# Kernel tuning notes

Hardware: AMD Instinct MI355X
Metric: run time of the kernel (lower is better)

The kernel has to match this reference:

```python
import jax, jax.numpy as jnp
import numpy as np

N = 20000       # nodes
E = 262144      # edges
DA, DV, DD = 128, 64, 32
R = 16          # CP rank of TensorProds
NRAD = 8        # radial basis size (hardcoded 8 in module)
R0 = 5.0        # cutoff radius r0


def setup_inputs() -> dict:
    key = jax.random.key(0)
    ks = jax.random.split(key, 13)
    nrm = lambda k, shape, fan: jax.random.normal(k, shape, jnp.float32) / np.sqrt(fan)
    return {
        'r_ij': jax.random.normal(ks[0], (E, 3), jnp.float32),
        'x_a': jax.random.normal(ks[1], (N, DA), jnp.float32),
        'x_v': jax.random.normal(ks[2], (N, DV, 3), jnp.float32),
        'x_d': jax.random.normal(ks[3], (N, DD, 3, 3), jnp.float32),
        'W1_a': nrm(ks[4], (3, R, DA), DA),   # tp_000, tp_011, tp_022 (rank-0 input)
        'W1_v': nrm(ks[5], (4, R, DV), DV),   # tp_101, tp_110, tp_112, tp_121
        'W1_d': nrm(ks[6], (4, R, DD), DD),   # tp_202, tp_211, tp_220, tp_222
        'W2': nrm(ks[7], (11, R, NRAD), NRAD),  # radial-side proj for all 11 TPs
        'Wo_a': nrm(ks[8], (3, DA, R), R),    # outputs of tp_000, tp_110, tp_220
        'Wo_v': nrm(ks[9], (4, DV, R), R),    # outputs of tp_011, tp_101, tp_121, tp_211
        'Wo_d': nrm(ks[10], (4, DD, R), R),   # outputs of tp_022, tp_112, tp_202, tp_222
        'src': jax.random.randint(ks[11], (E,), 0, N),
        'dst': jax.random.randint(ks[12], (E,), 0, N),
    }


def tens_sigmoid_vec(v, eps=1e-6):
    # direction-preserving bounded nonlinearity on rank-1 tensors
    n = jnp.linalg.norm(v, axis=-1, keepdims=True)
    return v * (2.0 * jax.nn.sigmoid(n) - 1.0) / (n + eps)


def _forward(r_ij, x_a, x_v, x_d, W1_a, W1_v, W1_d, W2, Wo_a, Wo_v, Wo_d, src, dst):
    n_nodes = x_a.shape[0]
    # radial_encode_edge(r, 8, r0)
    npi = jnp.pi * jnp.arange(NRAD, dtype=jnp.float32)
    x_sq = jnp.sum(r_ij * r_ij, -1) / R0                       # (E,)
    rad = jnp.cos(npi * jnp.sqrt(x_sq)[:, None]) * jax.nn.relu(1.0 - x_sq)[:, None]  # (E,8)
    rv = tens_sigmoid_vec(r_ij * (17.0 / R0))                  # (E,3)
    phi_a = rad                                                # (E,8)
    phi_v = rad[..., None] * rv[:, None, :]                    # (E,8,3)
    phi_d = rad[..., None, None] * rv[:, None, None, :] * rv[:, None, :, None]  # (E,8,3,3)
    # edges_read_dst: gather node features at destination nodes
    xa_j, xv_j, xd_j = x_a[dst], x_v[dst], x_d[dst]
    p1 = lambda W, x: jnp.einsum('rc,ec...->er...', W, x)      # channel->CP-rank proj
    outp = lambda Wo, t: jnp.einsum('dr,er...->ed...', Wo, t)  # CP-rank->channel proj
    p2a = lambda i: jnp.einsum('rc,ec->er', W2[i], phi_a)
    p2v = lambda i: jnp.einsum('rc,eci->eri', W2[i], phi_v)
    p2d = lambda i: jnp.einsum('rc,ecij->erij', W2[i], phi_d)
    # W2 index order: 000,110,220,011,101,121,211,022,112,202,222
    pa000, pa011, pa022 = p1(W1_a[0], xa_j), p1(W1_a[1], xa_j), p1(W1_a[2], xa_j)
    pv101, pv110, pv112, pv121 = (p1(W1_v[i], xv_j) for i in range(4))
    pd202, pd211, pd220, pd222 = (p1(W1_d[i], xd_j) for i in range(4))
    psi_a = (outp(Wo_a[0], pa000 * p2a(0))
             + outp(Wo_a[1], jnp.einsum('eri,eri->er', pv110, p2v(1)))
             + outp(Wo_a[2], jnp.einsum('erij,erij->er', pd220, p2d(2))))
    psi_v = (outp(Wo_v[0], pa011[..., None] * p2v(3))
             + outp(Wo_v[1], pv101 * p2a(4)[..., None])
             + outp(Wo_v[2], jnp.einsum('eri,erij->erj', pv121, p2d(5)))
             + outp(Wo_v[3], jnp.einsum('erij,erj->eri', pd211, p2v(6))))
    psi_d = (outp(Wo_d[0], pa022[..., None, None] * p2d(7))
             + outp(Wo_d[1], jnp.einsum('eri,erj->erij', pv112, p2v(8)))
             + outp(Wo_d[2], pd202 * p2a(9)[..., None, None])
             + outp(Wo_d[3], jnp.einsum('erik,erkj->erij', pd222, p2d(10))))
    # edges_reduce_src: scatter-add messages to source nodes
    B_a = jax.ops.segment_sum(psi_a, src, num_segments=n_nodes)
    B_v = jax.ops.segment_sum(psi_v, src, num_segments=n_nodes)
    B_d = jax.ops.segment_sum(psi_d, src, num_segments=n_nodes)
    return (B_a, B_v, B_d)


def reference(r_ij, x_a, x_v, x_d, W1_a, W1_v, W1_d, W2, Wo_a, Wo_v, Wo_d, src, dst):
    return _forward(r_ij, x_a, x_v, x_d, W1_a, W1_v, W1_d, W2, Wo_a, Wo_v, Wo_d, src, dst)
```

## Files before the change

### kernel.cpp

```cpp
#include <hip/hip_runtime.h>
#include <hip/hip_bf16.h>
#include <math.h>

#define PI_F 3.14159265358979323846f
#define R0_F 5.0f


static __device__ __forceinline__ float dot4(float4 a, float4 b) {
  return a.x * b.x + a.y * b.y + a.z * b.z + a.w * b.w;
}

__global__ __launch_bounds__(256) void node_proj_kernel(
    const float* __restrict__ x_a, const float* __restrict__ x_v, const float* __restrict__ x_d,
    const float* __restrict__ W1_a, const float* __restrict__ W1_v, const float* __restrict__ W1_d,
    float* __restrict__ P, int N)
{
  __shared__ float S[12352];
  const int tid = threadIdx.x;
  const int lane = tid & 63;
  const int wu = __builtin_amdgcn_readfirstlane(tid >> 6);
  const int n0 = blockIdx.x * 64;
  const int nrem = min(N - n0, 64);
  const int phase = blockIdx.y;

  if (phase == 0) {
    for (int idx4 = tid; idx4 < nrem * 32; idx4 += 256) {
      int n = idx4 >> 5, c4 = idx4 & 31;
      float4 v = ((const float4*)(x_a + (size_t)(n0 + n) * 128))[c4];
      float* d = &S[n * 129 + c4 * 4];
      d[0] = v.x; d[1] = v.y; d[2] = v.z; d[3] = v.w;
    }
    __syncthreads();
    float acc[12];
    #pragma unroll
    for (int q = 0; q < 12; q++) acc[q] = 0.0f;
    const float* xrow = &S[lane * 129];
    for (int c0 = 0; c0 < 128; c0 += 16) {
      float xr[16];
      #pragma unroll
      for (int j = 0; j < 16; j++) xr[j] = xrow[c0 + j];
      #pragma unroll
      for (int q = 0; q < 12; q++) {
        int o = wu * 12 + q;
        const float* wp = W1_a + (o >> 4) * 2048 + (o & 15) * 128 + c0;
        float s = 0.0f;
        #pragma unroll
        for (int j = 0; j < 16; j++) s += wp[j] * xr[j];
        acc[q] += s;
      }
    }
    __syncthreads();
    #pragma unroll
    for (int q = 0; q < 12; q++) S[lane * 49 + wu * 12 + q] = acc[q];
    __syncthreads();
    for (int u = tid; u < nrem * 12; u += 256) {
      int n = u / 12, m4 = u - n * 12;
      const float* s = &S[n * 49 + m4 * 4];
      ((float4*)(P + (size_t)(n0 + n) * 816))[m4] = make_float4(s[0], s[1], s[2], s[3]);
    }
  } else if (phase == 1) {
    for (int idx4 = tid; idx4 < nrem * 48; idx4 += 256) {
      int n = idx4 / 48, m4 = idx4 - n * 48;
      float4 v = ((const float4*)(x_v + (size_t)(n0 + n) * 192))[m4];
      float* d = &S[n * 193 + m4 * 4];
      d[0] = v.x; d[1] = v.y; d[2] = v.z; d[3] = v.w;
    }
    __syncthreads();
    float acc[16][3];
    #pragma unroll
    for (int r = 0; r < 16; r++)
      #pragma unroll
      for (int i = 0; i < 3; i++) acc[r][i] = 0.0f;
    const float* xrow = &S[lane * 193];
    for (int c0 = 0; c0 < 64; c0 += 16) {
      float xr[16][3];
      #pragma unroll
      for (int j = 0; j < 16; j++) {
        xr[j][0] = xrow[(c0 + j) * 3 + 0];
        xr[j][1] = xrow[(c0 + j) * 3 + 1];
        xr[j][2] = xrow[(c0 + j) * 3 + 2];
      }
      #pragma unroll
      for (int r = 0; r < 16; r++) {
        const float* wp = W1_v + wu * 1024 + r * 64 + c0;
        #pragma unroll
        for (int j = 0; j < 16; j++) {
          float w = wp[j];
          acc[r][0] += w * xr[j][0];
          acc[r][1] += w * xr[j][1];
          acc[r][2] += w * xr[j][2];
        }
      }
    }
    __syncthreads();
    #pragma unroll
    for (int r = 0; r < 16; r++)
      #pragma unroll
      for (int i = 0; i < 3; i++)
        S[lane * 193 + wu * 48 + r * 3 + i] = acc[r][i];
    __syncthreads();
    for (int u = tid; u < nrem * 48; u += 256) {
      int n = u / 48, m4 = u - n * 48;
      const float* s = &S[n * 193 + m4 * 4];
      ((float4*)(P + (size_t)(n0 + n) * 816 + 48))[m4] = make_float4(s[0], s[1], s[2], s[3]);
    }
  } else if (phase == 2) {
    for (int idx = tid; idx < nrem * 160; idx += 256) {
      int n = idx / 160, m = idx - n * 160, c = m / 5, ij = m - c * 5;
      S[n * 161 + m] = x_d[(size_t)(n0 + n) * 288 + c * 9 + ij];
    }
    __syncthreads();
    float acc[16][5];
    #pragma unroll
    for (int r = 0; r < 16; r++)
      #pragma unroll
      for (int t = 0; t < 5; t++) acc[r][t] = 0.0f;
    const float* xrow = &S[lane * 161];
    for (int c0 = 0; c0 < 32; c0 += 8) {
      float xr[8][5];
      #pragma unroll
      for (int j = 0; j < 8; j++)
        #pragma unroll
        for (int t = 0; t < 5; t++) xr[j][t] = xrow[(c0 + j) * 5 + t];
      #pragma unroll
      for (int r = 0; r < 16; r++) {
        const float* wp = W1_d + wu * 512 + r * 32 + c0;
        #pragma unroll
        for (int j = 0; j < 8; j++) {
          float w = wp[j];
          #pragma unroll
          for (int t = 0; t < 5; t++) acc[r][t] += w * xr[j][t];
        }
      }
    }
    #pragma unroll
    for (int h = 0; h < 2; h++) {
      __syncthreads();
      if ((lane >> 5) == h) {
        int l5 = lane & 31;
        #pragma unroll
        for (int r = 0; r < 16; r++)
          #pragma unroll
          for (int t = 0; t < 5; t++)
            S[l5 * 321 + wu * 80 + r * 5 + t] = acc[r][t];
      }
      __syncthreads();
      int nbase = h * 32;
      int cnt = min(nrem - nbase, 32);
      for (int u = tid; u < cnt * 320; u += 256) {
        int n = u / 320, m = u - n * 320;
        int kk = m / 80, mm = m - kk * 80, rr = mm / 5, t = mm - rr * 5;
        P[(size_t)(n0 + nbase + n) * 816 + 240 + kk * 144 + 9 * rr + t] = S[n * 321 + m];
      }
    }
  } else {
    for (int idx = tid; idx < nrem * 128; idx += 256) {
      int n = idx >> 7, m = idx & 127, c = m >> 2, t = m & 3;
      S[n * 129 + m] = x_d[(size_t)(n0 + n) * 288 + c * 9 + 5 + t];
    }
    __syncthreads();
    float acc[16][4];
    #pragma unroll
    for (int r = 0; r < 16; r++)
      #pragma unroll
      for (int t = 0; t < 4; t++) acc[r][t] = 0.0f;
    const float* xrow = &S[lane * 129];
    for (int c0 = 0; c0 < 32; c0 += 8) {
      float xr[8][4];
      #pragma unroll
      for (int j = 0; j < 8; j++)
        #pragma unroll
        for (int t = 0; t < 4; t++) xr[j][t] = xrow[(c0 + j) * 4 + t];
      #pragma unroll
      for (int r = 0; r < 16; r++) {
        const float* wp = W1_d + wu * 512 + r * 32 + c0;
        #pragma unroll
        for (int j = 0; j < 8; j++) {
          float w = wp[j];
          #pragma unroll
          for (int t = 0; t < 4; t++) acc[r][t] += w * xr[j][t];
        }
      }
    }
    #pragma unroll
    for (int h = 0; h < 2; h++) {
      __syncthreads();
      if ((lane >> 5) == h) {
        int l5 = lane & 31;
        #pragma unroll
        for (int r = 0; r < 16; r++)
          #pragma unroll
          for (int t = 0; t < 4; t++)
            S[l5 * 257 + wu * 64 + r * 4 + t] = acc[r][t];
      }
      __syncthreads();
      int nbase = h * 32;
      int cnt = min(nrem - nbase, 32);
      for (int u = tid; u < cnt * 256; u += 256) {
        int n = u >> 8, m = u & 255;
        int kk = m >> 6, mm = m & 63, rr = mm >> 2, t = mm & 3;
        P[(size_t)(n0 + nbase + n) * 816 + 240 + kk * 144 + 9 * rr + 5 + t] = S[n * 257 + m];
      }
    }
  }
}

__global__ void hist_kernel(const int* __restrict__ src, int* __restrict__ counts, int E) {
  int e = blockIdx.x * 256 + threadIdx.x;
  if (e < E) atomicAdd(&counts[src[e]], 1);
}

__global__ __launch_bounds__(1024) void scan_kernel(
    const int* __restrict__ counts, int* __restrict__ offs, int* __restrict__ cursor,
    int N, int E)
{
  __shared__ int part[1024];
  int tid = threadIdx.x;
  int chunk = (N + 1023) / 1024;
  int lo = tid * chunk, hi = min(lo + chunk, N);
  int s = 0;
  for (int i = lo; i < hi; i++) s += counts[i];
  part[tid] = s;
  __syncthreads();
  for (int off = 1; off < 1024; off <<= 1) {
    int v = (tid >= off) ? part[tid - off] : 0;
    __syncthreads();
    part[tid] += v;
    __syncthreads();
  }
  int run = part[tid] - s;
  for (int i = lo; i < hi; i++) { offs[i] = run; cursor[i] = run; run += counts[i]; }
  if (tid == 0) offs[N] = E;
}

__global__ void scatter_kernel(const int* __restrict__ src, int* __restrict__ cursor,
                               int* __restrict__ eidx, int E) {
  int e = blockIdx.x * 256 + threadIdx.x;
  if (e < E) { int p = atomicAdd(&cursor[src[e]], 1); eidx[p] = e; }
}

__global__ __launch_bounds__(256) void node_gather_kernel(
    const float* __restrict__ r_ij, const int* __restrict__ dst,
    const int* __restrict__ offs, const int* __restrict__ eidx,
    const float* __restrict__ Pg, const float* __restrict__ W2,
    const float* __restrict__ Wo_a, const float* __restrict__ Wo_v, const float* __restrict__ Wo_d,
    float* __restrict__ out, int N)
{
  __shared__ __align__(16) float Sall[5120];
  const int wid = threadIdx.x >> 6;
  const int lane = threadIdx.x & 63;
  const int n = blockIdx.x * 4 + wid;
  if (n >= N) return;
  float* S = Sall + wid * 1280;
  float4* S4 = (float4*)S;
  const int off = offs[n], deg = offs[n + 1] - off;

  int aP[12], aQ[12], aF[12];
  unsigned typm = 0;
  #pragma unroll
  for (int p = 0; p < 3; p++) {
    int t = lane + 64 * p;
    int k = t / 48, m = t - 48 * k, jj = m >> 4, r = m & 15;
    int q_ = 816 + (3 + k) * 16 + r;
    int P_, F_;
    if (k == 0)      { P_ = 16 + r;              F_ = 992 + jj; }
    else if (k == 1) { P_ = 48 + 3 * r + jj;     F_ = 995; }
    else if (k == 2) { P_ = 192 + 3 * r;         F_ = 992 + jj; typm |= 1u << p; }
    else             { P_ = 384 + 9 * r + 3 * jj; F_ = 995;     typm |= 1u << p; }
    aP[p] = P_; aQ[p] = q_; aF[p] = F_;
  }
  #pragma unroll
  for (int p = 0; p < 9; p++) {
    int u = lane + 64 * p;
    int s = u / 144, m = u - 144 * s, ij = m >> 4, r = m & 15;
    int i = ij / 3, jj = ij - 3 * i;
    int P_, F_, q_;
    if (s == 0)      { P_ = 32 + r;              q_ = 112 + r; F_ = 996 + ij; }
    else if (s == 1) { P_ = 144 + 3 * r + i;     q_ = 128 + r; F_ = 992 + jj; }
    else if (s == 2) { P_ = 240 + 9 * r + ij;    q_ = 144 + r; F_ = 995; }
    else             { P_ = 672 + 9 * r + 3 * i; q_ = 160 + r; F_ = 992 + jj; typm |= 1u << (3 + p); }
    aP[3 + p] = P_; aQ[3 + p] = 816 + q_; aF[3 + p] = F_;
  }
  const int ak = lane >> 4, ar = lane & 15;

  float4 wqa[3], wqb[3];
  #pragma unroll
  for (int p = 0; p < 3; p++) {
    int tq = lane + 64 * p; if (tq > 175) tq = 175;
    const float4* w = (const float4*)(W2 + tq * 8);
    wqa[p] = w[0]; wqb[p] = w[1];
  }

  float accA = 0.0f, acc[12];
  #pragma unroll
  for (int p = 0; p < 12; p++) acc[p] = 0.0f;

  float4 pb0 = {}, pb1 = {}, pb2 = {}, pb3 = {};
  const int l3 = 192 + (lane < 12 ? lane : 0);

  for (int base = 0; base < deg; base += 64) {
    int cnt = min(deg - base, 64);
    if (lane < cnt) {
      int e = eidx[off + base + lane];
      float a = r_ij[3 * (size_t)e], b = r_ij[3 * (size_t)e + 1], c = r_ij[3 * (size_t)e + 2];
      S4[252 + lane] = make_float4(a, b, c, __int_as_float(dst[e]));
    }
    {
      float4 me = S4[252];
      if (me.x * me.x + me.y * me.y + me.z * me.z < 5.0f) {
        const float4* Pp = (const float4*)(Pg + (size_t)__float_as_int(me.w) * 816);
        pb0 = Pp[lane]; pb1 = Pp[64 + lane]; pb2 = Pp[128 + lane]; pb3 = Pp[l3];
      }
    }
    for (int t = 0; t < cnt; t++) {
      float4 me = S4[252 + t];
      float r0 = me.x, r1 = me.y, r2 = me.z;
      float rr = r0 * r0 + r1 * r1 + r2 * r2;
      bool live = rr < 5.0f;
      float rv0 = 0, rv1 = 0, rv2 = 0;
      if (live) {
        float x_sq = rr * (1.0f / R0_F);
        float env = 1.0f - x_sq;
        float v0 = r0 * (17.0f / R0_F), v1 = r1 * (17.0f / R0_F), v2 = r2 * (17.0f / R0_F);
        float nn = sqrtf(v0 * v0 + v1 * v1 + v2 * v2);
        float sig = 2.0f / (1.0f + __expf(-nn)) - 1.0f;
        float sc = sig / (nn + 1e-6f);
        rv0 = v0 * sc; rv1 = v1 * sc; rv2 = v2 * sc;
        float rad[8];
        {
          float c1 = __cosf(PI_F * sqrtf(x_sq));
          float two_c1 = 2.0f * c1, cm2 = 1.0f, cm1 = c1;
          rad[0] = env; rad[1] = c1 * env;
          #pragma unroll
          for (int k = 2; k < 8; k++) { float c = two_c1 * cm1 - cm2; rad[k] = c * env; cm2 = cm1; cm1 = c; }
        }
        float4 ra = make_float4(rad[0], rad[1], rad[2], rad[3]);
        float4 rb = make_float4(rad[4], rad[5], rad[6], rad[7]);
        S4[lane] = pb0; S4[64 + lane] = pb1; S4[128 + lane] = pb2;
        if (lane < 12) S4[192 + lane] = pb3;
        S[816 + lane] = dot4(wqa[0], ra) + dot4(wqb[0], rb);
        S[880 + lane] = dot4(wqa[1], ra) + dot4(wqb[1], rb);
        if (lane < 48) S[944 + lane] = dot4(wqa[2], ra) + dot4(wqb[2], rb);
        if (lane < 4) S[992 + lane] = (lane == 0) ? rv0 : (lane == 1) ? rv1 : (lane == 2) ? rv2 : 1.0f;
        if (lane >= 4 && lane < 13) {
          int ij = lane - 4, i = ij / 3, j = ij - 3 * i;
          float a = (i == 0) ? rv0 : (i == 1) ? rv1 : rv2;
          float b = (j == 0) ? rv0 : (j == 1) ? rv1 : rv2;
          S[992 + lane] = a * b;
        }
      }
      if (t + 1 < cnt) {
        float4 m2 = S4[252 + t + 1];
        if (m2.x * m2.x + m2.y * m2.y + m2.z * m2.z < 5.0f) {
          const float4* Pp = (const float4*)(Pg + (size_t)__float_as_int(m2.w) * 816);
          pb0 = Pp[lane]; pb1 = Pp[64 + lane]; pb2 = Pp[128 + lane]; pb3 = Pp[l3];
        }
      }
      if (live) {
        if (lane < 48) {
          float v;
          if (ak == 0)      v = S[ar] * S[816 + ar];
          else if (ak == 1) v = (S[96 + 3 * ar] * rv0 + S[97 + 3 * ar] * rv1 + S[98 + 3 * ar] * rv2) * S[832 + ar];
          else {
            int b = 528 + 9 * ar;
            float o = (S[b] * rv0 + S[b + 3] * rv1 + S[b + 6] * rv2) * rv0
                    + (S[b + 1] * rv0 + S[b + 4] * rv1 + S[b + 7] * rv2) * rv1
                    + (S[b + 2] * rv0 + S[b + 5] * rv1 + S[b + 8] * rv2) * rv2;
            v = o * S[848 + ar];
          }
          accA += v;
        }
        #pragma unroll
        for (int p = 0; p < 12; p++) {
          float pv;
          if (typm & (1u << p)) pv = S[aP[p]] * rv0 + S[aP[p] + 1] * rv1 + S[aP[p] + 2] * rv2;
          else                  pv = S[aP[p]];
          acc[p] += pv * S[aQ[p]] * S[aF[p]];
        }
      }
    }
  }

  if (lane < 48) S[lane] = accA;
  #pragma unroll
  for (int p = 0; p < 3; p++) S[48 + lane + 64 * p] = acc[p];
  #pragma unroll
  for (int p = 0; p < 9; p++) {
    int u = lane + 64 * p;
    int s = u / 144, m = u - 144 * s, ij = m >> 4, r = m & 15;
    S[240 + s * 180 + ij * 20 + r] = acc[3 + p];
  }

  const size_t baseV = (size_t)N * 128;
  const size_t baseD = (size_t)N * 320;

  #pragma unroll
  for (int h = 0; h < 2; h++) {
    int c = lane + 64 * h;
    float a_ = 0.0f;
    #pragma unroll
    for (int k = 0; k < 3; k++) {
      const float4* w = (const float4*)(Wo_a + k * 2048 + c * 16);
      const float4* A4 = (const float4*)(&S[k * 16]);
      #pragma unroll
      for (int cc = 0; cc < 4; cc++) a_ += dot4(w[cc], A4[cc]);
    }
    out[(size_t)n * 128 + c] = a_;
  }
  {
    float o0 = 0, o1 = 0, o2 = 0;
    #pragma unroll
    for (int k = 0; k < 4; k++) {
      const float4* w = (const float4*)(Wo_v + k * 1024 + lane * 16);
      float4 w0 = w[0], w1 = w[1], w2 = w[2], w3 = w[3];
      #pragma unroll
      for (int j = 0; j < 3; j++) {
        const float4* A4 = (const float4*)(&S[48 + k * 48 + j * 16]);
        float v = dot4(w0, A4[0]) + dot4(w1, A4[1]) + dot4(w2, A4[2]) + dot4(w3, A4[3]);
        if (j == 0) o0 += v; else if (j == 1) o1 += v; else o2 += v;
      }
    }
    size_t ov = baseV + (size_t)n * 192 + lane * 3;
    out[ov] = o0; out[ov + 1] = o1; out[ov + 2] = o2;
  }
  #pragma unroll
  for (int p = 0; p < 5; p++) {
    int t = lane + 64 * p;
    if (t < 288) {
      int d = t / 9, ij = t - 9 * d;
      float a_ = 0.0f;
      #pragma unroll
      for (int s = 0; s < 4; s++) {
        const float4* w = (const float4*)(Wo_d + s * 512 + d * 16);
        const float4* A4 = (const float4*)(&S[240 + s * 180 + ij * 20]);
        a_ += dot4(w[0], A4[0]) + dot4(w[1], A4[1]) + dot4(w[2], A4[2]) + dot4(w[3], A4[3]);
      }
      out[baseD + (size_t)n * 288 + t] = a_;
    }
  }
}

extern "C" void kernel_launch(void* const* d_in, const int* in_sizes, int n_in,
                              void* d_out, int out_size, void* d_ws, size_t ws_size,
                              hipStream_t stream) {
  const float* r_ij = (const float*)d_in[0];
  const float* x_a  = (const float*)d_in[1];
  const float* x_v  = (const float*)d_in[2];
  const float* x_d  = (const float*)d_in[3];
  const float* W1_a = (const float*)d_in[4];
  const float* W1_v = (const float*)d_in[5];
  const float* W1_d = (const float*)d_in[6];
  const float* W2   = (const float*)d_in[7];
  const float* Wo_a = (const float*)d_in[8];
  const float* Wo_v = (const float*)d_in[9];
  const float* Wo_d = (const float*)d_in[10];
  const int*  src   = (const int*)d_in[11];
  const int*  dst   = (const int*)d_in[12];

  const int E = in_sizes[0] / 3;
  const int N = in_sizes[1] / 128;

  float* P    = (float*)d_ws;
  int* counts = (int*)(P + (size_t)N * 816);
  int* offs   = counts + N;
  int* cursor = offs + N + 1;
  int* eidx   = cursor + N;

  hipMemsetAsync(counts, 0, sizeof(int) * (size_t)N, stream);

  hist_kernel<<<(E + 255) / 256, 256, 0, stream>>>(src, counts, E);
  scan_kernel<<<1, 1024, 0, stream>>>(counts, offs, cursor, N, E);
  scatter_kernel<<<(E + 255) / 256, 256, 0, stream>>>(src, cursor, eidx, E);
  dim3 g1((N + 63) / 64, 4);
  node_proj_kernel<<<g1, 256, 0, stream>>>(x_a, x_v, x_d, W1_a, W1_v, W1_d, P, N);
  node_gather_kernel<<<(N + 3) / 4, 256, 0, stream>>>(r_ij, dst, offs, eidx, P, W2,
                                                      Wo_a, Wo_v, Wo_d, (float*)d_out, N);
}
```

Before: 437.6 us.

## Precompute edge radial features per chunk and double-buffer LDS edge state

The per-edge radial basis, the squashed direction vector and the liveness test are now computed once per 64-edge chunk, with each lane handling one edge, and staged in LDS. Previously the whole wavefront recomputed them serially for every edge. The inner loop is unrolled by two with ping-pong LDS buffers for the gathered node projections and radial weights, and the next node gather is prefetched two edges ahead. In exchange, edges beyond the cutoff are no longer skipped: they are processed with zero radial weights, which adds arithmetic. The per-block LDS footprint more than doubles, which may lower occupancy.

New measurement: 484.4 us. +10.7%, slower.

```diff
diff --git a/kernel.cpp b/kernel.cpp
--- a/kernel.cpp
+++ b/kernel.cpp
@@ -239,6 +239,62 @@
   if (e < E) { int p = atomicAdd(&cursor[src[e]], 1); eidx[p] = e; }
 }
 
+#define EDGE_STEP(T, SB, QB, TB, SBN4, QBN, TBN)                               \
+  {                                                                            \
+    const int t_ = (T);                                                        \
+    float4 sc0 = S4[520 + t_ * 3];                                             \
+    float rv0 = sc0.x, rv1 = sc0.y, rv2 = sc0.z;                               \
+    if (lane < 48) {                                                           \
+      float v;                                                                 \
+      if (ak == 0)      v = S[(SB) + ar] * S[(QB) + ar];                       \
+      else if (ak == 1) v = (S[(SB) + 96 + 3 * ar] * rv0 + S[(SB) + 97 + 3 * ar] * rv1 + S[(SB) + 98 + 3 * ar] * rv2) * S[(QB) + 16 + ar]; \
+      else {                                                                   \
+        int b_ = (SB) + 528 + 9 * ar;                                          \
+        float o = (S[b_] * rv0 + S[b_ + 3] * rv1 + S[b_ + 6] * rv2) * rv0      \
+                + (S[b_ + 1] * rv0 + S[b_ + 4] * rv1 + S[b_ + 7] * rv2) * rv1  \
+                + (S[b_ + 2] * rv0 + S[b_ + 5] * rv1 + S[b_ + 8] * rv2) * rv2; \
+        v = o * S[(QB) + 32 + ar];                                             \
+      }                                                                        \
+      accA += v;                                                               \
+    }                                                                          \
+    _Pragma("unroll")                                                          \
+    for (int p = 0; p < 12; p++) {                                             \
+      float pv;                                                                \
+      if (typm & (1u << p)) pv = S[(SB) + aP[p]] * rv0 + S[(SB) + aP[p] + 1] * rv1 + S[(SB) + aP[p] + 2] * rv2; \
+      else                  pv = S[(SB) + aP[p]];                              \
+      acc[p] += pv * S[(QB) + aQ[p]] * S[(TB) + aF[p]];                        \
+    }                                                                          \
+    if (t_ + 1 < cnt) {                                                        \
+      if (dln >= 0) {                                                          \
+        S4[(SBN4) + lane] = pb0; S4[(SBN4) + 64 + lane] = pb1;                 \
+        S4[(SBN4) + 128 + lane] = pb2;                                         \
+        if (lane < 12) S4[(SBN4) + 192 + lane] = pb3;                          \
+      }                                                                        \
+      float4 s1 = S4[520 + (t_ + 1) * 3 + 1], s2 = S4[520 + (t_ + 1) * 3 + 2]; \
+      S[(QBN) + lane] = dot4(wqa[0], s1) + dot4(wqb[0], s2);                   \
+      S[(QBN) + 64 + lane] = dot4(wqa[1], s1) + dot4(wqb[1], s2);              \
+      if (lane < 48) S[(QBN) + 128 + lane] = dot4(wqa[2], s1) + dot4(wqb[2], s2); \
+      float4 nx0 = S4[520 + (t_ + 1) * 3];                                     \
+      if (lane < 13) {                                                         \
+        float tv;                                                              \
+        if (lane < 4) tv = (lane == 0) ? nx0.x : (lane == 1) ? nx0.y : (lane == 2) ? nx0.z : 1.0f; \
+        else { int ij_ = lane - 4, i_ = ij_ / 3, j_ = ij_ - 3 * i_;            \
+               float av = (i_ == 0) ? nx0.x : (i_ == 1) ? nx0.y : nx0.z;       \
+               float bv = (j_ == 0) ? nx0.x : (j_ == 1) ? nx0.y : nx0.z;       \
+               tv = av * bv; }                                                 \
+        S[(TBN) + lane] = tv;                                                  \
+      }                                                                        \
+    }                                                                          \
+    if (t_ + 2 < cnt) {                                                        \
+      int dl2 = Si[2016 + t_ + 2];                                             \
+      if (dl2 >= 0) {                                                          \
+        const float4* Pp = (const float4*)(Pg + (size_t)dl2 * 816);            \
+        pb0 = Pp[lane]; pb1 = Pp[64 + lane]; pb2 = Pp[128 + lane]; pb3 = Pp[l3]; \
+      }                                                                        \
+      dln = dl2;                                                               \
+    } else dln = -1;                                                           \
+  }
+
 __global__ __launch_bounds__(256) void node_gather_kernel(
     const float* __restrict__ r_ij, const int* __restrict__ dst,
     const int* __restrict__ offs, const int* __restrict__ eidx,
@@ -246,13 +302,14 @@
     const float* __restrict__ Wo_a, const float* __restrict__ Wo_v, const float* __restrict__ Wo_d,
     float* __restrict__ out, int N)
 {
-  __shared__ __align__(16) float Sall[5120];
+  __shared__ __align__(16) float Sall[11392];
   const int wid = threadIdx.x >> 6;
   const int lane = threadIdx.x & 63;
   const int n = blockIdx.x * 4 + wid;
   if (n >= N) return;
-  float* S = Sall + wid * 1280;
+  float* S = Sall + wid * 2848;
   float4* S4 = (float4*)S;
+  int* Si = (int*)S;
   const int off = offs[n], deg = offs[n + 1] - off;
 
   int aP[12], aQ[12], aF[12];
@@ -261,12 +318,12 @@
   for (int p = 0; p < 3; p++) {
     int t = lane + 64 * p;
     int k = t / 48, m = t - 48 * k, jj = m >> 4, r = m & 15;
-    int q_ = 816 + (3 + k) * 16 + r;
+    int q_ = (3 + k) * 16 + r;
     int P_, F_;
-    if (k == 0)      { P_ = 16 + r;              F_ = 992 + jj; }
-    else if (k == 1) { P_ = 48 + 3 * r + jj;     F_ = 995; }
-    else if (k == 2) { P_ = 192 + 3 * r;         F_ = 992 + jj; typm |= 1u << p; }
-    else             { P_ = 384 + 9 * r + 3 * jj; F_ = 995;     typm |= 1u << p; }
+    if (k == 0)      { P_ = 16 + r;               F_ = jj; }
+    else if (k == 1) { P_ = 48 + 3 * r + jj;      F_ = 3;  }
+    else if (k == 2) { P_ = 192 + 3 * r;          F_ = jj; typm |= 1u << p; }
+    else             { P_ = 384 + 9 * r + 3 * jj; F_ = 3;  typm |= 1u << p; }
     aP[p] = P_; aQ[p] = q_; aF[p] = F_;
   }
   #pragma unroll
@@ -275,11 +332,11 @@
     int s = u / 144, m = u - 144 * s, ij = m >> 4, r = m & 15;
     int i = ij / 3, jj = ij - 3 * i;
     int P_, F_, q_;
-    if (s == 0)      { P_ = 32 + r;              q_ = 112 + r; F_ = 996 + ij; }
-    else if (s == 1) { P_ = 144 + 3 * r + i;     q_ = 128 + r; F_ = 992 + jj; }
-    else if (s == 2) { P_ = 240 + 9 * r + ij;    q_ = 144 + r; F_ = 995; }
-    else             { P_ = 672 + 9 * r + 3 * i; q_ = 160 + r; F_ = 992 + jj; typm |= 1u << (3 + p); }
-    aP[3 + p] = P_; aQ[3 + p] = 816 + q_; aF[3 + p] = F_;
+    if (s == 0)      { P_ = 32 + r;              q_ = 112 + r; F_ = 4 + ij; }
+    else if (s == 1) { P_ = 144 + 3 * r + i;     q_ = 128 + r; F_ = jj; }
+    else if (s == 2) { P_ = 240 + 9 * r + ij;    q_ = 144 + r; F_ = 3; }
+    else             { P_ = 672 + 9 * r + 3 * i; q_ = 160 + r; F_ = jj; typm |= 1u << (3 + p); }
+    aP[3 + p] = P_; aQ[3 + p] = q_; aF[3 + p] = F_;
   }
   const int ak = lane >> 4, ar = lane & 15;
 
@@ -297,86 +354,70 @@
 
   float4 pb0 = {}, pb1 = {}, pb2 = {}, pb3 = {};
   const int l3 = 192 + (lane < 12 ? lane : 0);
+  int dln = -1;
 
   for (int base = 0; base < deg; base += 64) {
-    int cnt = min(deg - base, 64);
+    const int cnt = min(deg - base, 64);
     if (lane < cnt) {
       int e = eidx[off + base + lane];
       float a = r_ij[3 * (size_t)e], b = r_ij[3 * (size_t)e + 1], c = r_ij[3 * (size_t)e + 2];
-      S4[252 + lane] = make_float4(a, b, c, __int_as_float(dst[e]));
+      int d = dst[e];
+      float rr = a * a + b * b + c * c;
+      bool live = rr < 5.0f;
+      float x_sq = rr * (1.0f / R0_F);
+      float env = fmaxf(1.0f - x_sq, 0.0f);
+      float v0 = a * (17.0f / R0_F), v1 = b * (17.0f / R0_F), v2 = c * (17.0f / R0_F);
+      float nn = sqrtf(v0 * v0 + v1 * v1 + v2 * v2);
+      float sig = 2.0f / (1.0f + __expf(-nn)) - 1.0f;
+      float scs = sig / (nn + 1e-6f);
+      float rv0 = v0 * scs, rv1 = v1 * scs, rv2 = v2 * scs;
+      float c1 = __cosf(PI_F * sqrtf(x_sq));
+      float two_c1 = 2.0f * c1, cm2 = 1.0f, cm1 = c1;
+      float rad[8];
+      rad[0] = env; rad[1] = c1 * env;
+      #pragma unroll
+      for (int k = 2; k < 8; k++) { float cc = two_c1 * cm1 - cm2; rad[k] = cc * env; cm2 = cm1; cm1 = cc; }
+      Si[2016 + lane] = live ? d : (d | (int)0x80000000);
+      S4[520 + lane * 3]     = make_float4(rv0, rv1, rv2, 0.0f);
+      S4[520 + lane * 3 + 1] = make_float4(rad[0], rad[1], rad[2], rad[3]);
+      S4[520 + lane * 3 + 2] = make_float4(rad[4], rad[5], rad[6], rad[7]);
     }
     {
-      float4 me = S4[252];
-      if (me.x * me.x + me.y * me.y + me.z * me.z < 5.0f) {
-        const float4* Pp = (const float4*)(Pg + (size_t)__float_as_int(me.w) * 816);
+      int d0 = Si[2016];
+      if (d0 >= 0) {
+        const float4* Pp = (const float4*)(Pg + (size_t)d0 * 816);
         pb0 = Pp[lane]; pb1 = Pp[64 + lane]; pb2 = Pp[128 + lane]; pb3 = Pp[l3];
       }
-    }
-    for (int t = 0; t < cnt; t++) {
-      float4 me = S4[252 + t];
-      float r0 = me.x, r1 = me.y, r2 = me.z;
-      float rr = r0 * r0 + r1 * r1 + r2 * r2;
-      bool live = rr < 5.0f;
-      float rv0 = 0, rv1 = 0, rv2 = 0;
-      if (live) {
-        float x_sq = rr * (1.0f / R0_F);
-        float env = 1.0f - x_sq;
-        float v0 = r0 * (17.0f / R0_F), v1 = r1 * (17.0f / R0_F), v2 = r2 * (17.0f / R0_F);
-        float nn = sqrtf(v0 * v0 + v1 * v1 + v2 * v2);
-        float sig = 2.0f / (1.0f + __expf(-nn)) - 1.0f;
-        float sc = sig / (nn + 1e-6f);
-        rv0 = v0 * sc; rv1 = v1 * sc; rv2 = v2 * sc;
-        float rad[8];
-        {
-          float c1 = __cosf(PI_F * sqrtf(x_sq));
-          float two_c1 = 2.0f * c1, cm2 = 1.0f, cm1 = c1;
-          rad[0] = env; rad[1] = c1 * env;
-          #pragma unroll
-          for (int k = 2; k < 8; k++) { float c = two_c1 * cm1 - cm2; rad[k] = c * env; cm2 = cm1; cm1 = c; }
-        }
-        float4 ra = make_float4(rad[0], rad[1], rad[2], rad[3]);
-        float4 rb = make_float4(rad[4], rad[5], rad[6], rad[7]);
-        S4[lane] = pb0; S4[64 + lane] = pb1; S4[128 + lane] = pb2;
-        if (lane < 12) S4[192 + lane] = pb3;
-        S[816 + lane] = dot4(wqa[0], ra) + dot4(wqb[0], rb);
-        S[880 + lane] = dot4(wqa[1], ra) + dot4(wqb[1], rb);
-        if (lane < 48) S[944 + lane] = dot4(wqa[2], ra) + dot4(wqb[2], rb);
-        if (lane < 4) S[992 + lane] = (lane == 0) ? rv0 : (lane == 1) ? rv1 : (lane == 2) ? rv2 : 1.0f;
-        if (lane >= 4 && lane < 13) {
-          int ij = lane - 4, i = ij / 3, j = ij - 3 * i;
-          float a = (i == 0) ? rv0 : (i == 1) ? rv1 : rv2;
-          float b = (j == 0) ? rv0 : (j == 1) ? rv1 : rv2;
-          S[992 + lane] = a * b;
-        }
-      }
-      if (t + 1 < cnt) {
-        float4 m2 = S4[252 + t + 1];
-        if (m2.x * m2.x + m2.y * m2.y + m2.z * m2.z < 5.0f) {
-          const float4* Pp = (const float4*)(Pg + (size_t)__float_as_int(m2.w) * 816);
+      float4 s1 = S4[521], s2 = S4[522];
+      S[1632 + lane] = dot4(wqa[0], s1) + dot4(wqb[0], s2);
+      S[1632 + 64 + lane] = dot4(wqa[1], s1) + dot4(wqb[1], s2);
+      if (lane < 48) S[1632 + 128 + lane] = dot4(wqa[2], s1) + dot4(wqb[2], s2);
+      float4 s0 = S4[520];
+      if (lane < 13) {
+        float tv;
+        if (lane < 4) tv = (lane == 0) ? s0.x : (lane == 1) ? s0.y : (lane == 2) ? s0.z : 1.0f;
+        else { int ij_ = lane - 4, i_ = ij_ / 3, j_ = ij_ - 3 * i_;
+               float av = (i_ == 0) ? s0.x : (i_ == 1) ? s0.y : s0.z;
+               float bv = (j_ == 0) ? s0.x : (j_ == 1) ? s0.y : s0.z;
+               tv = av * bv; }
+        S[1984 + lane] = tv;
+      }
+      S4[lane] = pb0; S4[64 + lane] = pb1; S4[128 + lane] = pb2;
+      if (lane < 12) S4[192 + lane] = pb3;
+      dln = -1;
+      if (cnt > 1) {
+        int d1 = Si[2016 + 1];
+        if (d1 >= 0) {
+          const float4* Pp = (const float4*)(Pg + (size_t)d1 * 816);
           pb0 = Pp[lane]; pb1 = Pp[64 + lane]; pb2 = Pp[128 + lane]; pb3 = Pp[l3];
         }
-      }
-      if (live) {
-        if (lane < 48) {
-          float v;
-          if (ak == 0)      v = S[ar] * S[816 + ar];
-          else if (ak == 1) v = (S[96 + 3 * ar] * rv0 + S[97 + 3 * ar] * rv1 + S[98 + 3 * ar] * rv2) * S[832 + ar];
-          else {
-            int b = 528 + 9 * ar;
-            float o = (S[b] * rv0 + S[b + 3] * rv1 + S[b + 6] * rv2) * rv0
-                    + (S[b + 1] * rv0 + S[b + 4] * rv1 + S[b + 7] * rv2) * rv1
-                    + (S[b + 2] * rv0 + S[b + 5] * rv1 + S[b + 8] * rv2) * rv2;
-            v = o * S[848 + ar];
-          }
-          accA += v;
-        }
-        #pragma unroll
-        for (int p = 0; p < 12; p++) {
-          float pv;
-          if (typm & (1u << p)) pv = S[aP[p]] * rv0 + S[aP[p] + 1] * rv1 + S[aP[p] + 2] * rv2;
-          else                  pv = S[aP[p]];
-          acc[p] += pv * S[aQ[p]] * S[aF[p]];
-        }
+        dln = d1;
+      }
+    }
+    for (int tt = 0; tt < cnt; tt += 2) {
+      EDGE_STEP(tt, 0, 1632, 1984, 204, 1808, 2000)
+      if (tt + 1 < cnt) {
+        EDGE_STEP(tt + 1, 816, 1808, 2000, 0, 1632, 1984)
       }
     }
   }
```

## Compact live edges per chunk and precompute edge geometry in parallel across lanes

Applied to the files above, without the earlier changes.

Each 64-edge chunk now computes its radial basis and normalized direction vectors in parallel, one edge per lane, and uses a ballot and prefix popcount to compact only in-cutoff edges into shared memory. The serial per-edge loop then runs only over live edges and no longer recomputes transcendentals with the whole wavefront. The radial projection staging for the next edge is pipelined alongside the gather prefetch two edges ahead. Shared memory per block grows from about 20 KB to about 30 KB, which may lower occupancy.

New measurement: 456.7 us. 1.04x slower.

```diff
diff --git a/kernel.cpp b/kernel.cpp
--- a/kernel.cpp
+++ b/kernel.cpp
@@ -246,13 +246,14 @@
     const float* __restrict__ Wo_a, const float* __restrict__ Wo_v, const float* __restrict__ Wo_d,
     float* __restrict__ out, int N)
 {
-  __shared__ __align__(16) float Sall[5120];
+  __shared__ __align__(16) float Sall[7488];
   const int wid = threadIdx.x >> 6;
   const int lane = threadIdx.x & 63;
   const int n = blockIdx.x * 4 + wid;
   if (n >= N) return;
-  float* S = Sall + wid * 1280;
+  float* S = Sall + wid * 1872;
   float4* S4 = (float4*)S;
+  int* Si = (int*)S;
   const int off = offs[n], deg = offs[n + 1] - off;
 
   int aP[12], aQ[12], aF[12];
@@ -299,84 +300,111 @@
   const int l3 = 192 + (lane < 12 ? lane : 0);
 
   for (int base = 0; base < deg; base += 64) {
-    int cnt = min(deg - base, 64);
+    const int cnt = min(deg - base, 64);
+    bool live = false;
+    float a = 0, b = 0, c = 0;
+    int d = 0;
     if (lane < cnt) {
       int e = eidx[off + base + lane];
-      float a = r_ij[3 * (size_t)e], b = r_ij[3 * (size_t)e + 1], c = r_ij[3 * (size_t)e + 2];
-      S4[252 + lane] = make_float4(a, b, c, __int_as_float(dst[e]));
-    }
+      a = r_ij[3 * (size_t)e]; b = r_ij[3 * (size_t)e + 1]; c = r_ij[3 * (size_t)e + 2];
+      d = dst[e];
+      live = (a * a + b * b + c * c) < 5.0f;
+    }
+    unsigned long long mb = __ballot(live);
+    const int cl = __popcll(mb);
+    if (live) {
+      int pos = __popcll(mb & ((1ull << lane) - 1ull));
+      float rr = a * a + b * b + c * c;
+      float x_sq = rr * (1.0f / R0_F);
+      float env = 1.0f - x_sq;
+      float v0 = a * (17.0f / R0_F), v1 = b * (17.0f / R0_F), v2 = c * (17.0f / R0_F);
+      float nn = sqrtf(v0 * v0 + v1 * v1 + v2 * v2);
+      float sig = 2.0f / (1.0f + __expf(-nn)) - 1.0f;
+      float scs = sig / (nn + 1e-6f);
+      float rv0 = v0 * scs, rv1 = v1 * scs, rv2 = v2 * scs;
+      float c1 = __cosf(PI_F * sqrtf(x_sq));
+      float two_c1 = 2.0f * c1, cm2 = 1.0f, cm1 = c1;
+      float rad[8];
+      rad[0] = env; rad[1] = c1 * env;
+      #pragma unroll
+      for (int k = 2; k < 8; k++) { float cc = two_c1 * cm1 - cm2; rad[k] = cc * env; cm2 = cm1; cm1 = cc; }
+      Si[1008 + pos] = d;
+      S4[268 + 3 * pos]     = make_float4(rv0, rv1, rv2, 0.0f);
+      S4[268 + 3 * pos + 1] = make_float4(rad[0], rad[1], rad[2], rad[3]);
+      S4[268 + 3 * pos + 2] = make_float4(rad[4], rad[5], rad[6], rad[7]);
+    }
+    if (cl == 0) continue;
     {
-      float4 me = S4[252];
-      if (me.x * me.x + me.y * me.y + me.z * me.z < 5.0f) {
-        const float4* Pp = (const float4*)(Pg + (size_t)__float_as_int(me.w) * 816);
-        pb0 = Pp[lane]; pb1 = Pp[64 + lane]; pb2 = Pp[128 + lane]; pb3 = Pp[l3];
-      }
-    }
-    for (int t = 0; t < cnt; t++) {
-      float4 me = S4[252 + t];
-      float r0 = me.x, r1 = me.y, r2 = me.z;
-      float rr = r0 * r0 + r1 * r1 + r2 * r2;
-      bool live = rr < 5.0f;
-      float rv0 = 0, rv1 = 0, rv2 = 0;
-      if (live) {
-        float x_sq = rr * (1.0f / R0_F);
-        float env = 1.0f - x_sq;
-        float v0 = r0 * (17.0f / R0_F), v1 = r1 * (17.0f / R0_F), v2 = r2 * (17.0f / R0_F);
-        float nn = sqrtf(v0 * v0 + v1 * v1 + v2 * v2);
-        float sig = 2.0f / (1.0f + __expf(-nn)) - 1.0f;
-        float sc = sig / (nn + 1e-6f);
-        rv0 = v0 * sc; rv1 = v1 * sc; rv2 = v2 * sc;
-        float rad[8];
-        {
-          float c1 = __cosf(PI_F * sqrtf(x_sq));
-          float two_c1 = 2.0f * c1, cm2 = 1.0f, cm1 = c1;
-          rad[0] = env; rad[1] = c1 * env;
-          #pragma unroll
-          for (int k = 2; k < 8; k++) { float c = two_c1 * cm1 - cm2; rad[k] = c * env; cm2 = cm1; cm1 = c; }
+      int d0 = Si[1008];
+      const float4* Pp = (const float4*)(Pg + (size_t)d0 * 816);
+      pb0 = Pp[lane]; pb1 = Pp[64 + lane]; pb2 = Pp[128 + lane]; pb3 = Pp[l3];
+      S4[lane] = pb0; S4[64 + lane] = pb1; S4[128 + lane] = pb2;
+      if (lane < 12) S4[192 + lane] = pb3;
+      float4 s1 = S4[269], s2 = S4[270];
+      S[816 + lane] = dot4(wqa[0], s1) + dot4(wqb[0], s2);
+      S[880 + lane] = dot4(wqa[1], s1) + dot4(wqb[1], s2);
+      if (lane < 48) S[944 + lane] = dot4(wqa[2], s1) + dot4(wqb[2], s2);
+      float4 s0 = S4[268];
+      if (lane < 13) {
+        float tv;
+        if (lane < 4) tv = (lane == 0) ? s0.x : (lane == 1) ? s0.y : (lane == 2) ? s0.z : 1.0f;
+        else { int ij_ = lane - 4, i_ = ij_ / 3, j_ = ij_ - 3 * i_;
+               float av = (i_ == 0) ? s0.x : (i_ == 1) ? s0.y : s0.z;
+               float bv = (j_ == 0) ? s0.x : (j_ == 1) ? s0.y : s0.z;
+               tv = av * bv; }
+        S[992 + lane] = tv;
+      }
+      if (cl > 1) {
+        int d1 = Si[1009];
+        const float4* Pq = (const float4*)(Pg + (size_t)d1 * 816);
+        pb0 = Pq[lane]; pb1 = Pq[64 + lane]; pb2 = Pq[128 + lane]; pb3 = Pq[l3];
+      }
+    }
+    for (int t = 0; t < cl; t++) {
+      float4 sc0 = S4[268 + 3 * t];
+      float rv0 = sc0.x, rv1 = sc0.y, rv2 = sc0.z;
+      if (lane < 48) {
+        float v;
+        if (ak == 0)      v = S[ar] * S[816 + ar];
+        else if (ak == 1) v = (S[96 + 3 * ar] * rv0 + S[97 + 3 * ar] * rv1 + S[98 + 3 * ar] * rv2) * S[832 + ar];
+        else {
+          int bb = 528 + 9 * ar;
+          float o = (S[bb] * rv0 + S[bb + 3] * rv1 + S[bb + 6] * rv2) * rv0
+                  + (S[bb + 1] * rv0 + S[bb + 4] * rv1 + S[bb + 7] * rv2) * rv1
+                  + (S[bb + 2] * rv0 + S[bb + 5] * rv1 + S[bb + 8] * rv2) * rv2;
+          v = o * S[848 + ar];
         }
-        float4 ra = make_float4(rad[0], rad[1], rad[2], rad[3]);
-        float4 rb = make_float4(rad[4], rad[5], rad[6], rad[7]);
+        accA += v;
+      }
+      #pragma unroll
+      for (int p = 0; p < 12; p++) {
+        float pv;
+        if (typm & (1u << p)) pv = S[aP[p]] * rv0 + S[aP[p] + 1] * rv1 + S[aP[p] + 2] * rv2;
+        else                  pv = S[aP[p]];
+        acc[p] += pv * S[aQ[p]] * S[aF[p]];
+      }
+      if (t + 1 < cl) {
         S4[lane] = pb0; S4[64 + lane] = pb1; S4[128 + lane] = pb2;
         if (lane < 12) S4[192 + lane] = pb3;
-        S[816 + lane] = dot4(wqa[0], ra) + dot4(wqb[0], rb);
-        S[880 + lane] = dot4(wqa[1], ra) + dot4(wqb[1], rb);
-        if (lane < 48) S[944 + lane] = dot4(wqa[2], ra) + dot4(wqb[2], rb);
-        if (lane < 4) S[992 + lane] = (lane == 0) ? rv0 : (lane == 1) ? rv1 : (lane == 2) ? rv2 : 1.0f;
-        if (lane >= 4 && lane < 13) {
-          int ij = lane - 4, i = ij / 3, j = ij - 3 * i;
-          float a = (i == 0) ? rv0 : (i == 1) ? rv1 : rv2;
-          float b = (j == 0) ? rv0 : (j == 1) ? rv1 : rv2;
-          S[992 + lane] = a * b;
+        float4 s1 = S4[268 + 3 * (t + 1) + 1], s2 = S4[268 + 3 * (t + 1) + 2];
+        S[816 + lane] = dot4(wqa[0], s1) + dot4(wqb[0], s2);
+        S[880 + lane] = dot4(wqa[1], s1) + dot4(wqb[1], s2);
+        if (lane < 48) S[944 + lane] = dot4(wqa[2], s1) + dot4(wqb[2], s2);
+        float4 nx0 = S4[268 + 3 * (t + 1)];
+        if (lane < 13) {
+          float tv;
+          if (lane < 4) tv = (lane == 0) ? nx0.x : (lane == 1) ? nx0.y : (lane == 2) ? nx0.z : 1.0f;
+          else { int ij_ = lane - 4, i_ = ij_ / 3, j_ = ij_ - 3 * i_;
+                 float av = (i_ == 0) ? nx0.x : (i_ == 1) ? nx0.y : nx0.z;
+                 float bv = (j_ == 0) ? nx0.x : (j_ == 1) ? nx0.y : nx0.z;
+                 tv = av * bv; }
+          S[992 + lane] = tv;
         }
       }
-      if (t + 1 < cnt) {
-        float4 m2 = S4[252 + t + 1];
-        if (m2.x * m2.x + m2.y * m2.y + m2.z * m2.z < 5.0f) {
-          const float4* Pp = (const float4*)(Pg + (size_t)__float_as_int(m2.w) * 816);
-          pb0 = Pp[lane]; pb1 = Pp[64 + lane]; pb2 = Pp[128 + lane]; pb3 = Pp[l3];
-        }
-      }
-      if (live) {
-        if (lane < 48) {
-          float v;
-          if (ak == 0)      v = S[ar] * S[816 + ar];
-          else if (ak == 1) v = (S[96 + 3 * ar] * rv0 + S[97 + 3 * ar] * rv1 + S[98 + 3 * ar] * rv2) * S[832 + ar];
-          else {
-            int b = 528 + 9 * ar;
-            float o = (S[b] * rv0 + S[b + 3] * rv1 + S[b + 6] * rv2) * rv0
-                    + (S[b + 1] * rv0 + S[b + 4] * rv1 + S[b + 7] * rv2) * rv1
-                    + (S[b + 2] * rv0 + S[b + 5] * rv1 + S[b + 8] * rv2) * rv2;
-            v = o * S[848 + ar];
-          }
-          accA += v;
-        }
-        #pragma unroll
-        for (int p = 0; p < 12; p++) {
-          float pv;
-          if (typm & (1u << p)) pv = S[aP[p]] * rv0 + S[aP[p] + 1] * rv1 + S[aP[p] + 2] * rv2;
-          else                  pv = S[aP[p]];
-          acc[p] += pv * S[aQ[p]] * S[aF[p]];
-        }
+      if (t + 2 < cl) {
+        int d2 = Si[1008 + t + 2];
+        const float4* Pp = (const float4*)(Pg + (size_t)d2 * 816);
+        pb0 = Pp[lane]; pb1 = Pp[64 + lane]; pb2 = Pp[128 + lane]; pb3 = Pp[l3];
       }
     }
   }
```
